# Optimization experiments

Hardware: AMD Instinct MI355X
Metric: run time of the kernel (lower is better)

Reference implementation:

```python
import jax, jax.numpy as jnp
import numpy as np

N_M, N_E = 100_000, 50_000      # materials / elements node counts
FM, FE, H = 256, 64, 128        # raw feature dims, hidden_channels
E, EL = 1_000_000, 250_000      # message edges per direction, label edges per decoder


def setup_inputs() -> dict:
    key = jax.random.key(0)
    ks = jax.random.split(key, 40)

    def w(i, shape):
        fan_in = shape[0]
        return jax.random.normal(ks[i], shape, jnp.float32) / np.sqrt(fan_in)

    inp = {
        "x_materials": jax.random.normal(ks[0], (N_M, FM), jnp.float32),
        "x_elements": jax.random.normal(ks[1], (N_E, FE), jnp.float32),
        # message-passing edges: materials->elements and elements->materials
        "src_m2e": jax.random.randint(ks[2], (E,), 0, N_M),
        "dst_m2e": jax.random.randint(ks[3], (E,), 0, N_E),
        "src_e2m": jax.random.randint(ks[4], (E,), 0, N_E),
        "dst_e2m": jax.random.randint(ks[5], (E,), 0, N_M),
        # supervision (edge_label_index) per decoder
        "lbl_src_m2e": jax.random.randint(ks[6], (EL,), 0, N_M),
        "lbl_dst_m2e": jax.random.randint(ks[7], (EL,), 0, N_E),
        "lbl_src_e2m": jax.random.randint(ks[8], (EL,), 0, N_E),
        "lbl_dst_e2m": jax.random.randint(ks[9], (EL,), 0, N_M),
        # input projections per node type
        "Wp_m": w(10, (FM, H)), "bp_m": jnp.zeros((H,), jnp.float32),
        "Wp_e": w(11, (FE, H)), "bp_e": jnp.zeros((H,), jnp.float32),
        # SAGEConv per edge type: lin_l (neighbor, with bias) + lin_r (root, no bias)
        "Wl_m2e": w(12, (H, H)), "bl_m2e": jnp.zeros((H,), jnp.float32), "Wr_m2e": w(13, (H, H)),
        "Wl_e2m": w(14, (H, H)), "bl_e2m": jnp.zeros((H,), jnp.float32), "Wr_e2m": w(15, (H, H)),
        # ffw linear per node type (to_hetero duplicates per node type)
        "Wffw_m": w(16, (H, H)), "bffw_m": jnp.zeros((H,), jnp.float32),
        "Wffw_e": w(17, (H, H)), "bffw_e": jnp.zeros((H,), jnp.float32),
        # output proj per node type
        "Wproj_m": w(18, (H, H)), "bproj_m": jnp.zeros((H,), jnp.float32),
        "Wproj_e": w(19, (H, H)), "bproj_e": jnp.zeros((H,), jnp.float32),
        # edge decoders (concat -> 2H -> 2H relu -> 1 -> sigmoid), one per edge type
        "Wmlp_m2e": w(20, (2 * H, 2 * H)), "bmlp_m2e": jnp.zeros((2 * H,), jnp.float32),
        "Wout_m2e": w(21, (2 * H, 1)), "bout_m2e": jnp.zeros((1,), jnp.float32),
        "Wmlp_e2m": w(22, (2 * H, 2 * H)), "bmlp_e2m": jnp.zeros((2 * H,), jnp.float32),
        "Wout_e2m": w(23, (2 * H, 1)), "bout_e2m": jnp.zeros((1,), jnp.float32),
    }
    return inp


def _sage(x_src, x_dst, src, dst, Wl, bl, Wr):
    """SAGEConv(aggr='mean'): W_l @ mean_{j in N(i)} x_j + b_l + W_r @ x_i."""
    n_dst = x_dst.shape[0]
    agg = jax.ops.segment_sum(x_src[src], dst, num_segments=n_dst)          # [n_dst, H]
    cnt = jax.ops.segment_sum(jnp.ones(src.shape, x_src.dtype), dst, num_segments=n_dst)
    mean = agg / jnp.maximum(cnt, 1.0)[:, None]
    return mean @ Wl + bl + x_dst @ Wr


def _decode(zs, zd, W1, b1, W2, b2):
    z = jnp.concatenate([zs, zd], axis=-1)                                  # [EL, 2H]
    z = jax.nn.relu(z @ W1 + b1)
    return jax.nn.sigmoid((z @ W2 + b2)[:, 0])                              # [EL]


def reference(x_materials, x_elements,
              src_m2e, dst_m2e, src_e2m, dst_e2m,
              lbl_src_m2e, lbl_dst_m2e, lbl_src_e2m, lbl_dst_e2m,
              Wp_m, bp_m, Wp_e, bp_e,
              Wl_m2e, bl_m2e, Wr_m2e, Wl_e2m, bl_e2m, Wr_e2m,
              Wffw_m, bffw_m, Wffw_e, bffw_e,
              Wproj_m, bproj_m, Wproj_e, bproj_e,
              Wmlp_m2e, bmlp_m2e, Wout_m2e, bout_m2e,
              Wmlp_e2m, bmlp_e2m, Wout_e2m, bout_e2m):
    # process_input_nodes: per-type projections
    z_m = x_materials @ Wp_m + bp_m
    z_e = x_elements @ Wp_e + bp_e
    # hetero SAGEConv layer (each node type has exactly one incoming edge type)
    h_m = jax.nn.relu(_sage(z_e, z_m, src_e2m, dst_e2m, Wl_e2m, bl_e2m, Wr_e2m))
    h_e = jax.nn.relu(_sage(z_m, z_e, src_m2e, dst_m2e, Wl_m2e, bl_m2e, Wr_m2e))
    # ffw layer per node type
    h_m = jax.nn.relu(h_m @ Wffw_m + bffw_m)
    h_e = jax.nn.relu(h_e @ Wffw_e + bffw_e)
    # output projection per node type
    h_m = h_m @ Wproj_m + bproj_m
    h_e = h_e @ Wproj_e + bproj_e
    # per-edge-type decoders on supervision edges
    out_m2e = _decode(h_m[lbl_src_m2e], h_e[lbl_dst_m2e], Wmlp_m2e, bmlp_m2e, Wout_m2e, bout_m2e)
    out_e2m = _decode(h_e[lbl_src_e2m], h_m[lbl_dst_e2m], Wmlp_e2m, bmlp_e2m, Wout_e2m, bout_e2m)
    return out_m2e, out_e2m
```

## Files before the change

### kernel.cpp

```cpp
#include <hip/hip_runtime.h>
#include <math.h>

#define N_M 100000
#define N_E 50000
#define FM 256
#define FE 64
#define H 128
#define NEDGE 1000000
#define NLBL 250000

#define BUCK 128
#define NB_M ((N_M + BUCK - 1) / BUCK)
#define NB_E ((N_E + BUCK - 1) / BUCK)
#define CAP_M 2048
#define CAP_E 4096
#define CHUNK 8192

typedef unsigned short u16;
typedef unsigned int u32;
typedef short bf16x8 __attribute__((ext_vector_type(8)));
typedef float f32x4  __attribute__((ext_vector_type(4)));
typedef u16 u16x8    __attribute__((ext_vector_type(8)));
typedef u16 u16x4    __attribute__((ext_vector_type(4)));

__device__ __forceinline__ u16 f2bf(float x) {
    unsigned u = __float_as_uint(x);
    u += 0x7FFF + ((u >> 16) & 1);
    return (u16)(u >> 16);
}
__device__ __forceinline__ float bf2f(u16 h) {
    return __uint_as_float(((unsigned)h) << 16);
}

#define NPACK 12
struct PackDesc { const float* src; u16* dst; int K, N; };
struct PackArgs { PackDesc d[NPACK]; };

__global__ __launch_bounds__(64)
void pack_kernel(PackArgs args)
{
    PackDesc pd = args.d[blockIdx.y];
    int KT = pd.K / 32, NT = pd.N / 16;
    int tile = blockIdx.x;
    if (tile >= KT * NT) return;
    int kt = tile / NT, nt = tile % NT;
    int l = threadIdx.x;
    u16* dst = pd.dst + ((size_t)tile * 64 + l) * 8;
    #pragma unroll
    for (int j = 0; j < 8; ++j) {
        float v = pd.src[(size_t)(kt * 32 + (l >> 4) * 8 + j) * pd.N + nt * 16 + (l & 15)];
        dst[j] = f2bf(v);
    }
}

template<int K, int N, bool HAS_A2, bool RELU, bool A_FP32, bool HAS_BIAS>
__global__ __launch_bounds__(256)
void mfma_gemm(const void* __restrict__ A1, const void* __restrict__ A2,
               const u16* __restrict__ W1p, const u16* __restrict__ W2p,
               const float* __restrict__ bias, u16* __restrict__ C, int M)
{
    constexpr int NT = N / 16, KT = K / 32;
    const int wid = threadIdx.x >> 6, lane = threadIdx.x & 63;
    const int row0 = blockIdx.x * 64 + wid * 16;
    if (row0 >= M) return;
    const int l15 = lane & 15, l4 = lane >> 4;

    f32x4 acc[NT];
    #pragma unroll
    for (int nt = 0; nt < NT; ++nt) acc[nt] = (f32x4){0.f, 0.f, 0.f, 0.f};

    const int npass = HAS_A2 ? 2 : 1;
    for (int pass = 0; pass < npass; ++pass) {
        const void* A = pass ? A2 : A1;
        const u16* Wp = pass ? W2p : W1p;
        #pragma unroll
        for (int kt = 0; kt < KT; ++kt) {
            bf16x8 a;
            if constexpr (A_FP32) {
                const float* ap = (const float*)A + (size_t)(row0 + l15) * K + kt * 32 + l4 * 8;
                float4 f0 = *(const float4*)ap;
                float4 f1 = *(const float4*)(ap + 4);
                a[0] = (short)f2bf(f0.x); a[1] = (short)f2bf(f0.y);
                a[2] = (short)f2bf(f0.z); a[3] = (short)f2bf(f0.w);
                a[4] = (short)f2bf(f1.x); a[5] = (short)f2bf(f1.y);
                a[6] = (short)f2bf(f1.z); a[7] = (short)f2bf(f1.w);
            } else {
                a = *(const bf16x8*)((const u16*)A + (size_t)(row0 + l15) * K + kt * 32 + l4 * 8);
            }
            #pragma unroll
            for (int nt = 0; nt < NT; ++nt) {
                bf16x8 b = *(const bf16x8*)(Wp + ((size_t)(kt * NT + nt) * 64 + lane) * 8);
                acc[nt] = __builtin_amdgcn_mfma_f32_16x16x32_bf16(a, b, acc[nt], 0, 0, 0);
            }
        }
    }

    #pragma unroll
    for (int nt = 0; nt < NT; ++nt) {
        #pragma unroll
        for (int r = 0; r < 4; ++r) {
            int row = row0 + l4 * 4 + r;
            int col = nt * 16 + l15;
            float v = acc[nt][r];
            if (HAS_BIAS) v += bias[col];
            if (RELU) v = fmaxf(v, 0.f);
            C[(size_t)row * N + col] = f2bf(v);
        }
    }
}

__global__ __launch_bounds__(1024)
void bucket2_kernel(const int* __restrict__ src_a, const int* __restrict__ dst_a,
                    const int* __restrict__ src_b, const int* __restrict__ dst_b,
                    u32* __restrict__ pairs_a, int* __restrict__ gcur_a,
                    u32* __restrict__ pairs_b, int* __restrict__ gcur_b)
{
    __shared__ int cnt[1024];
    __shared__ int gbase[1024];

    const int dir = blockIdx.y;
    const int* __restrict__ src = dir ? src_b : src_a;
    const int* __restrict__ dst = dir ? dst_b : dst_a;
    u32* __restrict__ pairs = dir ? pairs_b : pairs_a;
    int* __restrict__ gcur  = dir ? gcur_b : gcur_a;
    const int NB  = dir ? NB_E : NB_M;
    const int CAP = dir ? CAP_E : CAP_M;

    const int tid = threadIdx.x;
    const int e0 = blockIdx.x * CHUNK;
    const int e1 = min(e0 + CHUNK, NEDGE);

    cnt[tid] = 0;
    __syncthreads();

    int myd[CHUNK / 1024];
    int k = 0;
    for (int e = e0 + tid; e < e1; e += 1024, ++k) {
        int d = dst[e];
        myd[k] = d;
        atomicAdd(&cnt[d >> 7], 1);
    }
    __syncthreads();

    if (tid < NB) {
        int c = cnt[tid];
        gbase[tid] = (c > 0) ? atomicAdd(&gcur[tid], c) : 0;
        cnt[tid] = 0;
    }
    __syncthreads();

    k = 0;
    for (int e = e0 + tid; e < e1; e += 1024, ++k) {
        int d = myd[k];
        int b = d >> 7;
        int p = gbase[b] + atomicAdd(&cnt[b], 1);
        if (p < CAP)
            pairs[(size_t)b * CAP + p] = ((u32)(d & (BUCK - 1)) << 24) | (u32)src[e];
    }
}

__global__ __launch_bounds__(256)
void bucket_mean2_kernel(const u16* __restrict__ z_a, const u32* __restrict__ pairs_a,
                         const int* __restrict__ gcur_a, u16* __restrict__ out_a,
                         const u16* __restrict__ z_b, const u32* __restrict__ pairs_b,
                         const int* __restrict__ gcur_b, u16* __restrict__ out_b)
{
    __shared__ int loc_src[CAP_E];
    __shared__ int cnt[BUCK], seg[BUCK], cur[BUCK];

    const int dir = blockIdx.y;
    const int b = blockIdx.x;
    if (dir && b >= NB_E) return;

    const u16* __restrict__ z     = dir ? z_b : z_a;
    const u32* __restrict__ pairs = dir ? pairs_b : pairs_a;
    const int* __restrict__ gcur  = dir ? gcur_b : gcur_a;
    u16* __restrict__ outm        = dir ? out_b : out_a;
    const int cap     = dir ? CAP_E : CAP_M;
    const int n_nodes = dir ? N_E : N_M;

    const int tid = threadIdx.x;
    const int n = min(gcur[b], cap);
    const u32* __restrict__ pb = pairs + (size_t)b * cap;

    if (tid < BUCK) cnt[tid] = 0;
    __syncthreads();
    for (int e = tid; e < n; e += 256)
        atomicAdd(&cnt[pb[e] >> 24], 1);
    __syncthreads();

    int myc = (tid < BUCK) ? cnt[tid] : 0;
    if (tid < BUCK) seg[tid] = myc;
    __syncthreads();
    for (int off = 1; off < BUCK; off <<= 1) {
        int t = 0;
        if (tid < BUCK && tid >= off) t = seg[tid - off];
        __syncthreads();
        if (tid < BUCK && tid >= off) seg[tid] += t;
        __syncthreads();
    }
    if (tid < BUCK) { int ex = seg[tid] - myc; seg[tid] = ex; cur[tid] = ex; }
    __syncthreads();

    for (int e = tid; e < n; e += 256) {
        u32 pk = pb[e];
        int p = atomicAdd(&cur[pk >> 24], 1);
        loc_src[p] = (int)(pk & 0xFFFFFF);
    }
    __syncthreads();

    const int grp = tid >> 5, lane = tid & 31;
    for (int loc = grp; loc < BUCK; loc += 8) {
        int gnode = b * BUCK + loc;
        if (gnode >= n_nodes) continue;
        int s0 = seg[loc], c = cnt[loc];
        float4 accA = {0.f, 0.f, 0.f, 0.f};
        float4 accB = {0.f, 0.f, 0.f, 0.f};
        int i = 0;
        for (; i + 2 <= c; i += 2) {
            int sA = loc_src[s0 + i];
            int sB = loc_src[s0 + i + 1];
            u16x4 vA = *(const u16x4*)&z[(size_t)sA * H + lane * 4];
            u16x4 vB = *(const u16x4*)&z[(size_t)sB * H + lane * 4];
            accA.x += bf2f(vA[0]); accA.y += bf2f(vA[1]);
            accA.z += bf2f(vA[2]); accA.w += bf2f(vA[3]);
            accB.x += bf2f(vB[0]); accB.y += bf2f(vB[1]);
            accB.z += bf2f(vB[2]); accB.w += bf2f(vB[3]);
        }
        if (i < c) {
            int sA = loc_src[s0 + i];
            u16x4 vA = *(const u16x4*)&z[(size_t)sA * H + lane * 4];
            accA.x += bf2f(vA[0]); accA.y += bf2f(vA[1]);
            accA.z += bf2f(vA[2]); accA.w += bf2f(vA[3]);
        }
        accA.x += accB.x; accA.y += accB.y; accA.z += accB.z; accA.w += accB.w;
        float inv = 1.0f / fmaxf((float)c, 1.0f);
        u16x4 o;
        o[0] = f2bf(accA.x * inv); o[1] = f2bf(accA.y * inv);
        o[2] = f2bf(accA.z * inv); o[3] = f2bf(accA.w * inv);
        *(u16x4*)&outm[(size_t)gnode * H + lane * 4] = o;
    }
}

__global__ __launch_bounds__(256)
void edge_decode_mfma_kernel(const u16* __restrict__ hs, const u16* __restrict__ hd,
                             const int* __restrict__ lsrc, const int* __restrict__ ldst,
                             const u16* __restrict__ W1p,
                             const float* __restrict__ b1, const float* __restrict__ W2,
                             const float* __restrict__ b2, float* __restrict__ out)
{
    const int wid = threadIdx.x >> 6, lane = threadIdx.x & 63;
    const int l15 = lane & 15, l4 = lane >> 4;
    const int e0 = (blockIdx.x * 4 + wid) * 32;
    if (e0 >= NLBL) return;

    float b1v[16], w2v[16];
    #pragma unroll
    for (int nt = 0; nt < 16; ++nt) {
        b1v[nt] = b1[nt * 16 + l15];
        w2v[nt] = W2[nt * 16 + l15];
    }
    const float bout = b2[0];

    const int eA = min(e0 + l15, NLBL - 1);
    const int eB = min(e0 + 16 + l15, NLBL - 1);
    const int sA = lsrc[eA], dA = ldst[eA];
    const int sB = lsrc[eB], dB = ldst[eB];

    f32x4 acc0[16], acc1[16];
    #pragma unroll
    for (int nt = 0; nt < 16; ++nt) {
        acc0[nt] = (f32x4){0.f, 0.f, 0.f, 0.f};
        acc1[nt] = (f32x4){0.f, 0.f, 0.f, 0.f};
    }

    #pragma unroll
    for (int kt = 0; kt < 8; ++kt) {
        const int off = kt * 32 + l4 * 8;
        bf16x8 a0, a1;
        if (off < H) {
            a0 = *(const bf16x8*)&hs[(size_t)sA * H + off];
            a1 = *(const bf16x8*)&hs[(size_t)sB * H + off];
        } else {
            a0 = *(const bf16x8*)&hd[(size_t)dA * H + off - H];
            a1 = *(const bf16x8*)&hd[(size_t)dB * H + off - H];
        }
        #pragma unroll
        for (int nt = 0; nt < 16; ++nt) {
            bf16x8 b = *(const bf16x8*)&W1p[((size_t)(kt * 16 + nt) * 64 + lane) * 8];
            acc0[nt] = __builtin_amdgcn_mfma_f32_16x16x32_bf16(a0, b, acc0[nt], 0, 0, 0);
            acc1[nt] = __builtin_amdgcn_mfma_f32_16x16x32_bf16(a1, b, acc1[nt], 0, 0, 0);
        }
    }

    #pragma unroll
    for (int r = 0; r < 4; ++r) {
        float p0 = 0.f, p1 = 0.f;
        #pragma unroll
        for (int nt = 0; nt < 16; ++nt) {
            p0 += fmaxf(acc0[nt][r] + b1v[nt], 0.f) * w2v[nt];
            p1 += fmaxf(acc1[nt][r] + b1v[nt], 0.f) * w2v[nt];
        }
        p0 += __shfl_xor(p0, 1, 16); p0 += __shfl_xor(p0, 2, 16);
        p0 += __shfl_xor(p0, 4, 16); p0 += __shfl_xor(p0, 8, 16);
        p1 += __shfl_xor(p1, 1, 16); p1 += __shfl_xor(p1, 2, 16);
        p1 += __shfl_xor(p1, 4, 16); p1 += __shfl_xor(p1, 8, 16);
        if (l15 == 0) {
            int ea = e0 + l4 * 4 + r;
            int eb = ea + 16;
            if (ea < NLBL) out[ea] = 1.0f / (1.0f + expf(-(p0 + bout)));
            if (eb < NLBL) out[eb] = 1.0f / (1.0f + expf(-(p1 + bout)));
        }
    }
}

extern "C" void kernel_launch(void* const* d_in, const int* in_sizes, int n_in,
                              void* d_out, int out_size, void* d_ws, size_t ws_size,
                              hipStream_t stream)
{
    const float* x_m      = (const float*)d_in[0];
    const float* x_e      = (const float*)d_in[1];
    const int*   src_m2e  = (const int*)d_in[2];
    const int*   dst_m2e  = (const int*)d_in[3];
    const int*   src_e2m  = (const int*)d_in[4];
    const int*   dst_e2m  = (const int*)d_in[5];
    const int*   lsrc_m2e = (const int*)d_in[6];
    const int*   ldst_m2e = (const int*)d_in[7];
    const int*   lsrc_e2m = (const int*)d_in[8];
    const int*   ldst_e2m = (const int*)d_in[9];
    const float* Wp_m   = (const float*)d_in[10];
    const float* bp_m   = (const float*)d_in[11];
    const float* Wp_e   = (const float*)d_in[12];
    const float* bp_e   = (const float*)d_in[13];
    const float* Wl_m2e = (const float*)d_in[14];
    const float* bl_m2e = (const float*)d_in[15];
    const float* Wr_m2e = (const float*)d_in[16];
    const float* Wl_e2m = (const float*)d_in[17];
    const float* bl_e2m = (const float*)d_in[18];
    const float* Wr_e2m = (const float*)d_in[19];
    const float* Wffw_m = (const float*)d_in[20];
    const float* bffw_m = (const float*)d_in[21];
    const float* Wffw_e = (const float*)d_in[22];
    const float* bffw_e = (const float*)d_in[23];
    const float* Wproj_m = (const float*)d_in[24];
    const float* bproj_m = (const float*)d_in[25];
    const float* Wproj_e = (const float*)d_in[26];
    const float* bproj_e = (const float*)d_in[27];
    const float* Wmlp_m2e = (const float*)d_in[28];
    const float* bmlp_m2e = (const float*)d_in[29];
    const float* Wout_m2e = (const float*)d_in[30];
    const float* bout_m2e = (const float*)d_in[31];
    const float* Wmlp_e2m = (const float*)d_in[32];
    const float* bmlp_e2m = (const float*)d_in[33];
    const float* Wout_e2m = (const float*)d_in[34];
    const float* bout_e2m = (const float*)d_in[35];

    float* out = (float*)d_out;

    u16* B_m = (u16*)d_ws;
    u16* B_e = B_m + (size_t)N_M * H;
    u16* A_m = B_e + (size_t)N_E * H;
    u16* A_e = A_m + (size_t)N_M * H;
    u32* pairs_m = (u32*)(A_e + (size_t)N_E * H);
    u32* pairs_e = pairs_m + (size_t)NB_M * CAP_M;
    int* gcur_m  = (int*)(pairs_e + (size_t)NB_E * CAP_E);
    int* gcur_e  = gcur_m + NB_M;
    u16* pk = (u16*)(gcur_e + NB_E);
    u16* pWp_m   = pk;  pk += 256 * 128;
    u16* pWp_e   = pk;  pk += 64 * 128;
    u16* pWl_e2m = pk;  pk += 128 * 128;
    u16* pWr_e2m = pk;  pk += 128 * 128;
    u16* pWl_m2e = pk;  pk += 128 * 128;
    u16* pWr_m2e = pk;  pk += 128 * 128;
    u16* pWffw_m = pk;  pk += 128 * 128;
    u16* pWffw_e = pk;  pk += 128 * 128;
    u16* pWproj_m= pk;  pk += 128 * 128;
    u16* pWproj_e= pk;  pk += 128 * 128;
    u16* pW1_m2e = pk;  pk += 256 * 256;
    u16* pW1_e2m = pk;  pk += 256 * 256;

    dim3 blk(256);
    dim3 gm((N_M + 63) / 64), ge((N_E + 63) / 64);

    PackArgs pa;
    pa.d[0]  = { Wp_m,     pWp_m,    FM,  H };
    pa.d[1]  = { Wp_e,     pWp_e,    FE,  H };
    pa.d[2]  = { Wl_e2m,   pWl_e2m,  H,   H };
    pa.d[3]  = { Wr_e2m,   pWr_e2m,  H,   H };
    pa.d[4]  = { Wl_m2e,   pWl_m2e,  H,   H };
    pa.d[5]  = { Wr_m2e,   pWr_m2e,  H,   H };
    pa.d[6]  = { Wffw_m,   pWffw_m,  H,   H };
    pa.d[7]  = { Wffw_e,   pWffw_e,  H,   H };
    pa.d[8]  = { Wproj_m,  pWproj_m, H,   H };
    pa.d[9]  = { Wproj_e,  pWproj_e, H,   H };
    pa.d[10] = { Wmlp_m2e, pW1_m2e,  256, 256 };
    pa.d[11] = { Wmlp_e2m, pW1_e2m,  256, 256 };
    pack_kernel<<<dim3(128, NPACK), dim3(64), 0, stream>>>(pa);

    mfma_gemm<FM, H, false, false, true, true><<<gm, blk, 0, stream>>>(
        x_m, nullptr, pWp_m, nullptr, bp_m, A_m, N_M);
    mfma_gemm<FE, H, false, false, true, true><<<ge, blk, 0, stream>>>(
        x_e, nullptr, pWp_e, nullptr, bp_e, A_e, N_E);

    hipMemsetAsync(gcur_m, 0, sizeof(int) * (NB_M + NB_E), stream);
    const int nbk = (NEDGE + CHUNK - 1) / CHUNK;
    bucket2_kernel<<<dim3(nbk, 2), dim3(1024), 0, stream>>>(
        src_e2m, dst_e2m, src_m2e, dst_m2e,
        pairs_m, gcur_m, pairs_e, gcur_e);

    bucket_mean2_kernel<<<dim3(NB_M, 2), blk, 0, stream>>>(
        A_e, pairs_m, gcur_m, B_m,
        A_m, pairs_e, gcur_e, B_e);

    mfma_gemm<H, H, true, true, false, true><<<gm, blk, 0, stream>>>(
        B_m, A_m, pWl_e2m, pWr_e2m, bl_e2m, B_m, N_M);
    mfma_gemm<H, H, true, true, false, true><<<ge, blk, 0, stream>>>(
        B_e, A_e, pWl_m2e, pWr_m2e, bl_m2e, B_e, N_E);

    mfma_gemm<H, H, false, true, false, true><<<gm, blk, 0, stream>>>(
        B_m, nullptr, pWffw_m, nullptr, bffw_m, A_m, N_M);
    mfma_gemm<H, H, false, true, false, true><<<ge, blk, 0, stream>>>(
        B_e, nullptr, pWffw_e, nullptr, bffw_e, A_e, N_E);

    mfma_gemm<H, H, false, false, false, true><<<gm, blk, 0, stream>>>(
        A_m, nullptr, pWproj_m, nullptr, bproj_m, B_m, N_M);
    mfma_gemm<H, H, false, false, false, true><<<ge, blk, 0, stream>>>(
        A_e, nullptr, pWproj_e, nullptr, bproj_e, B_e, N_E);

    dim3 gdec((NLBL + 127) / 128);
    edge_decode_mfma_kernel<<<gdec, blk, 0, stream>>>(
        B_m, B_e, lsrc_m2e, ldst_m2e, pW1_m2e, bmlp_m2e, Wout_m2e, bout_m2e, out);
    edge_decode_mfma_kernel<<<gdec, blk, 0, stream>>>(
        B_e, B_m, lsrc_e2m, ldst_e2m, pW1_e2m, bmlp_e2m, Wout_e2m, bout_e2m, out + NLBL);
}
```

Measured before the change: 448.3 us.

## Fuse both edge decoders into one persistent kernel with LDS-staged W1

Replaces the two per-direction edge-decoder launches with one kernel that uses blockIdx.y to pick the direction. The grid is a persistent 256x2, and each wave loops over tiles of 32 edges. Each block first copies the full 128 KB packed W1 decoder weight into LDS, so the MFMA B operands come from shared memory instead of repeated global/L1 loads. The trade-off is that this large LDS footprint limits residency to about one 4-wave block per CU, which reduces the latency hiding available for the random row gathers.

```diff
diff --git a/kernel.cpp b/kernel.cpp
--- a/kernel.cpp
+++ b/kernel.cpp
@@ -243,16 +243,36 @@
 }
 
 __global__ __launch_bounds__(256)
-void edge_decode_mfma_kernel(const u16* __restrict__ hs, const u16* __restrict__ hd,
-                             const int* __restrict__ lsrc, const int* __restrict__ ldst,
-                             const u16* __restrict__ W1p,
-                             const float* __restrict__ b1, const float* __restrict__ W2,
-                             const float* __restrict__ b2, float* __restrict__ out)
-{
-    const int wid = threadIdx.x >> 6, lane = threadIdx.x & 63;
+void edge_decode_mfma2_kernel(const u16* __restrict__ B_m, const u16* __restrict__ B_e,
+                              const int* __restrict__ lsrc0, const int* __restrict__ ldst0,
+                              const int* __restrict__ lsrc1, const int* __restrict__ ldst1,
+                              const u16* __restrict__ W1p0, const u16* __restrict__ W1p1,
+                              const float* __restrict__ b1_0, const float* __restrict__ W2_0,
+                              const float* __restrict__ b2_0,
+                              const float* __restrict__ b1_1, const float* __restrict__ W2_1,
+                              const float* __restrict__ b2_1,
+                              float* __restrict__ out)
+{
+    extern __shared__ u16 w1s[];
+
+    const int dir = blockIdx.y;
+    const u16* __restrict__ hs   = dir ? B_e : B_m;
+    const u16* __restrict__ hd   = dir ? B_m : B_e;
+    const int* __restrict__ lsrc = dir ? lsrc1 : lsrc0;
+    const int* __restrict__ ldst = dir ? ldst1 : ldst0;
+    const u16* __restrict__ W1p  = dir ? W1p1 : W1p0;
+    const float* __restrict__ b1 = dir ? b1_1 : b1_0;
+    const float* __restrict__ W2 = dir ? W2_1 : W2_0;
+    const float bout             = dir ? b2_1[0] : b2_0[0];
+    float* __restrict__ outp     = out + (size_t)dir * NLBL;
+
+    const int tid = threadIdx.x;
+    const int wid = tid >> 6, lane = tid & 63;
     const int l15 = lane & 15, l4 = lane >> 4;
-    const int e0 = (blockIdx.x * 4 + wid) * 32;
-    if (e0 >= NLBL) return;
+
+    for (int i = tid; i < 256 * 256 / 8; i += 256)
+        ((u16x8*)w1s)[i] = ((const u16x8*)W1p)[i];
+    __syncthreads();
 
     float b1v[16], w2v[16];
     #pragma unroll
@@ -260,56 +280,59 @@
         b1v[nt] = b1[nt * 16 + l15];
         w2v[nt] = W2[nt * 16 + l15];
     }
-    const float bout = b2[0];
-
-    const int eA = min(e0 + l15, NLBL - 1);
-    const int eB = min(e0 + 16 + l15, NLBL - 1);
-    const int sA = lsrc[eA], dA = ldst[eA];
-    const int sB = lsrc[eB], dB = ldst[eB];
-
-    f32x4 acc0[16], acc1[16];
-    #pragma unroll
-    for (int nt = 0; nt < 16; ++nt) {
-        acc0[nt] = (f32x4){0.f, 0.f, 0.f, 0.f};
-        acc1[nt] = (f32x4){0.f, 0.f, 0.f, 0.f};
-    }
-
-    #pragma unroll
-    for (int kt = 0; kt < 8; ++kt) {
-        const int off = kt * 32 + l4 * 8;
-        bf16x8 a0, a1;
-        if (off < H) {
-            a0 = *(const bf16x8*)&hs[(size_t)sA * H + off];
-            a1 = *(const bf16x8*)&hs[(size_t)sB * H + off];
-        } else {
-            a0 = *(const bf16x8*)&hd[(size_t)dA * H + off - H];
-            a1 = *(const bf16x8*)&hd[(size_t)dB * H + off - H];
-        }
+
+    const int NTILES = (NLBL + 31) / 32;
+    for (int tile = blockIdx.x * 4 + wid; tile < NTILES; tile += gridDim.x * 4) {
+        const int e0 = tile * 32;
+        const int eA = min(e0 + l15, NLBL - 1);
+        const int eB = min(e0 + 16 + l15, NLBL - 1);
+        const int sA = lsrc[eA], dA = ldst[eA];
+        const int sB = lsrc[eB], dB = ldst[eB];
+
+        f32x4 acc0[16], acc1[16];
         #pragma unroll
         for (int nt = 0; nt < 16; ++nt) {
-            bf16x8 b = *(const bf16x8*)&W1p[((size_t)(kt * 16 + nt) * 64 + lane) * 8];
-            acc0[nt] = __builtin_amdgcn_mfma_f32_16x16x32_bf16(a0, b, acc0[nt], 0, 0, 0);
-            acc1[nt] = __builtin_amdgcn_mfma_f32_16x16x32_bf16(a1, b, acc1[nt], 0, 0, 0);
-        }
-    }
-
-    #pragma unroll
-    for (int r = 0; r < 4; ++r) {
-        float p0 = 0.f, p1 = 0.f;
+            acc0[nt] = (f32x4){0.f, 0.f, 0.f, 0.f};
+            acc1[nt] = (f32x4){0.f, 0.f, 0.f, 0.f};
+        }
+
         #pragma unroll
-        for (int nt = 0; nt < 16; ++nt) {
-            p0 += fmaxf(acc0[nt][r] + b1v[nt], 0.f) * w2v[nt];
-            p1 += fmaxf(acc1[nt][r] + b1v[nt], 0.f) * w2v[nt];
-        }
-        p0 += __shfl_xor(p0, 1, 16); p0 += __shfl_xor(p0, 2, 16);
-        p0 += __shfl_xor(p0, 4, 16); p0 += __shfl_xor(p0, 8, 16);
-        p1 += __shfl_xor(p1, 1, 16); p1 += __shfl_xor(p1, 2, 16);
-        p1 += __shfl_xor(p1, 4, 16); p1 += __shfl_xor(p1, 8, 16);
-        if (l15 == 0) {
-            int ea = e0 + l4 * 4 + r;
-            int eb = ea + 16;
-            if (ea < NLBL) out[ea] = 1.0f / (1.0f + expf(-(p0 + bout)));
-            if (eb < NLBL) out[eb] = 1.0f / (1.0f + expf(-(p1 + bout)));
+        for (int kt = 0; kt < 8; ++kt) {
+            const int off = kt * 32 + l4 * 8;
+            bf16x8 a0, a1;
+            if (off < H) {
+                a0 = *(const bf16x8*)&hs[(size_t)sA * H + off];
+                a1 = *(const bf16x8*)&hs[(size_t)sB * H + off];
+            } else {
+                a0 = *(const bf16x8*)&hd[(size_t)dA * H + off - H];
+                a1 = *(const bf16x8*)&hd[(size_t)dB * H + off - H];
+            }
+            #pragma unroll
+            for (int nt = 0; nt < 16; ++nt) {
+                bf16x8 b = *(const bf16x8*)&w1s[((kt * 16 + nt) * 64 + lane) * 8];
+                acc0[nt] = __builtin_amdgcn_mfma_f32_16x16x32_bf16(a0, b, acc0[nt], 0, 0, 0);
+                acc1[nt] = __builtin_amdgcn_mfma_f32_16x16x32_bf16(a1, b, acc1[nt], 0, 0, 0);
+            }
+        }
+
+        #pragma unroll
+        for (int r = 0; r < 4; ++r) {
+            float p0 = 0.f, p1 = 0.f;
+            #pragma unroll
+            for (int nt = 0; nt < 16; ++nt) {
+                p0 += fmaxf(acc0[nt][r] + b1v[nt], 0.f) * w2v[nt];
+                p1 += fmaxf(acc1[nt][r] + b1v[nt], 0.f) * w2v[nt];
+            }
+            p0 += __shfl_xor(p0, 1, 16); p0 += __shfl_xor(p0, 2, 16);
+            p0 += __shfl_xor(p0, 4, 16); p0 += __shfl_xor(p0, 8, 16);
+            p1 += __shfl_xor(p1, 1, 16); p1 += __shfl_xor(p1, 2, 16);
+            p1 += __shfl_xor(p1, 4, 16); p1 += __shfl_xor(p1, 8, 16);
+            if (l15 == 0) {
+                int ea = e0 + l4 * 4 + r;
+                int eb = ea + 16;
+                if (ea < NLBL) outp[ea] = 1.0f / (1.0f + expf(-(p0 + bout)));
+                if (eb < NLBL) outp[eb] = 1.0f / (1.0f + expf(-(p1 + bout)));
+            }
         }
     }
 }
@@ -427,9 +450,11 @@
     mfma_gemm<H, H, false, false, false, true><<<ge, blk, 0, stream>>>(
         A_e, nullptr, pWproj_e, nullptr, bproj_e, B_e, N_E);
 
-    dim3 gdec((NLBL + 127) / 128);
-    edge_decode_mfma_kernel<<<gdec, blk, 0, stream>>>(
-        B_m, B_e, lsrc_m2e, ldst_m2e, pW1_m2e, bmlp_m2e, Wout_m2e, bout_m2e, out);
-    edge_decode_mfma_kernel<<<gdec, blk, 0, stream>>>(
-        B_e, B_m, lsrc_e2m, ldst_e2m, pW1_e2m, bmlp_e2m, Wout_e2m, bout_e2m, out + NLBL);
-}
+    edge_decode_mfma2_kernel<<<dim3(256, 2), blk, 131072, stream>>>(
+        B_m, B_e,
+        lsrc_m2e, ldst_m2e, lsrc_e2m, ldst_e2m,
+        pW1_m2e, pW1_e2m,
+        bmlp_m2e, Wout_m2e, bout_m2e,
+        bmlp_e2m, Wout_e2m, bout_e2m,
+        out);
+}
```

Measured after the change: 616.6 us. 1.38x slower.
